# Kernel optimization log

Hardware: AMD Instinct MI355X
Metric: run time of the kernel (lower is better)

Reference implementation:

```python
import jax, jax.numpy as jnp
import numpy as np

NUM_HEADS = 16
HEAD_DIM = 128
D_MODEL = 2048
BATCH = 2
SEQ = 2048


def setup_inputs() -> dict:
    key = jax.random.key(0)
    ks = jax.random.split(key, 6)
    x = jax.random.normal(ks[0], (BATCH, SEQ, D_MODEL), dtype=jnp.float32)
    # RoPE tables (real/imag parts of freqs_cis), shape [S, HEAD_DIM//2]
    pos = jnp.arange(SEQ, dtype=jnp.float32)[:, None]
    inv_freq = 1.0 / (10000.0 ** (jnp.arange(0, HEAD_DIM, 2, dtype=jnp.float32) / HEAD_DIM))
    ang = pos * inv_freq[None, :]
    freq_cos = jnp.cos(ang)
    freq_sin = jnp.sin(ang)
    scale = 1.0 / np.sqrt(D_MODEL)
    wq = jax.random.normal(ks[1], (D_MODEL, NUM_HEADS * HEAD_DIM), dtype=jnp.float32) * scale
    wk = jax.random.normal(ks[2], (D_MODEL, NUM_HEADS * HEAD_DIM), dtype=jnp.float32) * scale
    wv = jax.random.normal(ks[3], (D_MODEL, NUM_HEADS * HEAD_DIM), dtype=jnp.float32) * scale
    wo = jax.random.normal(ks[4], (NUM_HEADS * HEAD_DIM, D_MODEL), dtype=jnp.float32) * scale
    return {"x": x, "freq_cos": freq_cos, "freq_sin": freq_sin,
            "wq": wq, "wk": wk, "wv": wv, "wo": wo}


def _rotate_half(t):
    half = t.shape[-1] // 2
    return jnp.concatenate([-t[..., half:], t[..., :half]], axis=-1)


def _apply_rope(q, k, freq_cos, freq_sin):
    # q, k: [B, H, S, D]; freq_cos/sin: [S_total, D//2]
    q = q.astype(jnp.float32)
    k = k.astype(jnp.float32)
    S = q.shape[2]
    cos = jnp.concatenate([freq_cos[:S], freq_cos[:S]], axis=-1)[None, None]  # [1,1,S,D]
    sin = jnp.concatenate([freq_sin[:S], freq_sin[:S]], axis=-1)[None, None]
    q_out = q * cos + _rotate_half(q) * sin
    k_out = k * cos + _rotate_half(k) * sin
    return q_out, k_out


def reference(x, freq_cos, freq_sin, wq, wk, wv, wo):
    B, S, D = x.shape
    H, hd = NUM_HEADS, HEAD_DIM
    q = (x @ wq).reshape(B, S, H, hd).transpose(0, 2, 1, 3)  # [B,H,S,hd]
    k = (x @ wk).reshape(B, S, H, hd).transpose(0, 2, 1, 3)
    v = (x @ wv).reshape(B, S, H, hd).transpose(0, 2, 1, 3)
    q, k = _apply_rope(q, k, freq_cos, freq_sin)
    # explicit causal attention (faithful to CPU/GPU path)
    logits = jnp.einsum('bhqd,bhkd->bhqk', q, k) / jnp.sqrt(jnp.float32(hd))
    mask = jnp.tril(jnp.ones((S, S), dtype=jnp.float32))
    logits = jnp.where(mask[None, None, :, :], logits, -1e10)
    weights = jax.nn.softmax(logits, axis=-1)
    out = jnp.einsum('bhqk,bhkd->bhqd', weights, v)  # [B,H,S,hd]
    out = out.transpose(0, 2, 1, 3).reshape(B, S, H * hd)
    return out @ wo
```

## Files before the change

kernel.cpp:

```cpp
#include <hip/hip_runtime.h>

typedef unsigned short u16;
typedef unsigned int u32;
typedef __attribute__((ext_vector_type(8))) short bf16x8;
typedef __attribute__((ext_vector_type(4))) short bf16x4;
typedef __attribute__((ext_vector_type(4))) float f32x4;

#define MFMA(a, b, c) __builtin_amdgcn_mfma_f32_16x16x32_bf16(a, b, c, 0, 0, 0)
#define ASYNC16(g, l)                                                        \
  __builtin_amdgcn_global_load_lds(                                          \
      (const __attribute__((address_space(1))) u32*)(g),                     \
      (__attribute__((address_space(3))) u32*)(l), 16, 0, 0)

__device__ __forceinline__ float b2f(u16 u) {
  union { u32 i; float f; } x; x.i = ((u32)u) << 16; return x.f;
}
__device__ __forceinline__ u16 f2b(float f) {
  union { float f; u32 i; } x; x.f = f;
  return (u16)((x.i + 0x7fff + ((x.i >> 16) & 1)) >> 16);
}
__device__ __forceinline__ f32x4 fzero4() { f32x4 z = {0.f, 0.f, 0.f, 0.f}; return z; }

__global__ __launch_bounds__(256) void cvt_x(const float* __restrict__ src,
                                             u16* __restrict__ dst) {
  const int i = (blockIdx.x * 256 + threadIdx.x) * 4;
  const f32x4 v = *(const f32x4*)(src + i);
  bf16x4 o;
  o[0] = (short)f2b(v[0]); o[1] = (short)f2b(v[1]);
  o[2] = (short)f2b(v[2]); o[3] = (short)f2b(v[3]);
  *(bf16x4*)(dst + i) = o;
}

__global__ __launch_bounds__(256) void wtrans_f32(const float* __restrict__ src,
                                                  u16* __restrict__ dst) {
  __shared__ u16 tile[64][65];
  const int k0 = blockIdx.y * 64, n0 = blockIdx.x * 64;
  const int t = threadIdx.x;
  const int tr = t >> 3, tc = t & 7;

#pragma unroll
  for (int hh = 0; hh < 2; ++hh) {
    const int k = tr + hh * 32;
    const float* p = src + (size_t)(k0 + k) * 2048 + n0 + tc * 8;
    const f32x4 a = *(const f32x4*)(p);
    const f32x4 b = *(const f32x4*)(p + 4);
#pragma unroll
    for (int j = 0; j < 4; ++j) tile[k][tc * 8 + j] = f2b(a[j]);
#pragma unroll
    for (int j = 0; j < 4; ++j) tile[k][tc * 8 + 4 + j] = f2b(b[j]);
  }
  __syncthreads();
#pragma unroll
  for (int hh = 0; hh < 2; ++hh) {
    const int n = tr + hh * 32;
    bf16x8 v;
#pragma unroll
    for (int j = 0; j < 8; ++j) v[j] = (short)tile[tc * 8 + j][n];
    *(bf16x8*)(dst + (size_t)(n0 + n) * 2048 + k0 + tc * 8) = v;
  }
}

__global__ __launch_bounds__(256) void wtrans3(const float* __restrict__ wq,
                                               const float* __restrict__ wk,
                                               const float* __restrict__ wv,
                                               u16* __restrict__ wTall) {
  __shared__ u16 tile[64][65];
  const int z = blockIdx.z;
  const float* src = (z == 0) ? wq : (z == 1) ? wk : wv;
  u16* dst = wTall + (size_t)z * 2048 * 2048;
  const int k0 = blockIdx.y * 64, n0 = blockIdx.x * 64;
  const int t = threadIdx.x;
  const int tr = t >> 3, tc = t & 7;

#pragma unroll
  for (int hh = 0; hh < 2; ++hh) {
    const int k = tr + hh * 32;
    const float* p = src + (size_t)(k0 + k) * 2048 + n0 + tc * 8;
    const f32x4 a = *(const f32x4*)(p);
    const f32x4 b = *(const f32x4*)(p + 4);
#pragma unroll
    for (int j = 0; j < 4; ++j) tile[k][tc * 8 + j] = f2b(a[j]);
#pragma unroll
    for (int j = 0; j < 4; ++j) tile[k][tc * 8 + 4 + j] = f2b(b[j]);
  }
  __syncthreads();
#pragma unroll
  for (int hh = 0; hh < 2; ++hh) {
    const int n = tr + hh * 32;
    bf16x8 v;
#pragma unroll
    for (int j = 0; j < 8; ++j) v[j] = (short)tile[tc * 8 + j][n];
    *(bf16x8*)(dst + (size_t)(n0 + n) * 2048 + k0 + tc * 8) = v;
  }
}

__device__ __forceinline__ void gemm_mainloop(const u16* __restrict__ A,
                                              const u16* __restrict__ Bt,
                                              int K, int m0, int n0,
                                              u16* lA, u16* lB,
                                              f32x4 acc[4][4]) {
  const int tid = threadIdx.x;
  const int lane = tid & 63;
  const int wave = tid >> 6;
  const int quad = lane >> 4;
  const int l16 = lane & 15;
  const int wr = wave >> 1, wc = wave & 1;

  const int srow = lane >> 2;
  const int scol = (lane & 3) * 8;
  const u16* ga0 = A + (size_t)(m0 + (wave * 2 + 0) * 16 + srow) * K + scol;
  const u16* ga1 = A + (size_t)(m0 + (wave * 2 + 1) * 16 + srow) * K + scol;
  const u16* gb0 = Bt + (size_t)(n0 + (wave * 2 + 0) * 16 + srow) * K + scol;
  const u16* gb1 = Bt + (size_t)(n0 + (wave * 2 + 1) * 16 + srow) * K + scol;
  u16* la0 = lA + (wave * 2 + 0) * 512;
  u16* la1 = lA + (wave * 2 + 1) * 512;
  u16* lb0 = lB + (wave * 2 + 0) * 512;
  u16* lb1 = lB + (wave * 2 + 1) * 512;

  for (int k0 = 0; k0 < K; k0 += 32) {
    ASYNC16(ga0 + k0, la0);
    ASYNC16(ga1 + k0, la1);
    ASYNC16(gb0 + k0, lb0);
    ASYNC16(gb1 + k0, lb1);
    __syncthreads();
    bf16x8 af[4], bfr[4];
#pragma unroll
    for (int mb = 0; mb < 4; ++mb)
      af[mb] = *(const bf16x8*)(lA + ((wr * 64 + mb * 16 + l16) * 32 + quad * 8));
#pragma unroll
    for (int nb = 0; nb < 4; ++nb)
      bfr[nb] = *(const bf16x8*)(lB + ((wc * 64 + nb * 16 + l16) * 32 + quad * 8));
#pragma unroll
    for (int mb = 0; mb < 4; ++mb)
#pragma unroll
      for (int nb = 0; nb < 4; ++nb)
        acc[mb][nb] = MFMA(af[mb], bfr[nb], acc[mb][nb]);
    __syncthreads();
  }
}

__global__ __launch_bounds__(256) void gemm_qkv(const u16* __restrict__ x,
                                                const u16* __restrict__ wT,
                                                u16* __restrict__ qkv) {
  __shared__ u16 lA[128 * 32];
  __shared__ u16 lB[128 * 32];
  f32x4 acc[4][4];
#pragma unroll
  for (int i = 0; i < 4; ++i)
#pragma unroll
    for (int j = 0; j < 4; ++j) acc[i][j] = fzero4();

  const int m0 = blockIdx.y * 128, n0 = blockIdx.x * 128;
  gemm_mainloop(x, wT, 2048, m0, n0, lA, lB, acc);

  const int lane = threadIdx.x & 63, wave = threadIdx.x >> 6;
  const int quad = lane >> 4, l16 = lane & 15;
  const int wr = wave >> 1, wc = wave & 1;
#pragma unroll
  for (int mb = 0; mb < 4; ++mb)
#pragma unroll
    for (int nb = 0; nb < 4; ++nb)
#pragma unroll
      for (int r = 0; r < 4; ++r) {
        const int row = m0 + wr * 64 + mb * 16 + quad * 4 + r;
        const int col = n0 + wc * 64 + nb * 16 + l16;
        const int b = row >> 11, s = row & 2047;
        const int which = col >> 11, rem = col & 2047;
        const int hh = rem >> 7, d = rem & 127;
        const size_t idx = (size_t)which * ((size_t)4096 * 2048) +
                           (((size_t)(b * 16 + hh) * 2048 + s) * 128 + d);
        qkv[idx] = f2b(acc[mb][nb][r]);
      }
}

__global__ __launch_bounds__(256) void gemm_out(const u16* __restrict__ Oin,
                                                const u16* __restrict__ woT,
                                                float* __restrict__ out) {
  __shared__ u16 lA[128 * 32];
  __shared__ u16 lB[128 * 32];
  f32x4 acc[4][4];
#pragma unroll
  for (int i = 0; i < 4; ++i)
#pragma unroll
    for (int j = 0; j < 4; ++j) acc[i][j] = fzero4();

  const int m0 = blockIdx.y * 128, n0 = blockIdx.x * 128;
  gemm_mainloop(Oin, woT, 2048, m0, n0, lA, lB, acc);

  const int lane = threadIdx.x & 63, wave = threadIdx.x >> 6;
  const int quad = lane >> 4, l16 = lane & 15;
  const int wr = wave >> 1, wc = wave & 1;
#pragma unroll
  for (int mb = 0; mb < 4; ++mb)
#pragma unroll
    for (int nb = 0; nb < 4; ++nb)
#pragma unroll
      for (int r = 0; r < 4; ++r) {
        const int row = m0 + wr * 64 + mb * 16 + quad * 4 + r;
        const int col = n0 + wc * 64 + nb * 16 + l16;
        out[(size_t)row * 2048 + col] = acc[mb][nb][r];
      }
}

__global__ __launch_bounds__(256) void rope_kernel(u16* __restrict__ Q,
                                                   u16* __restrict__ K,
                                                   const float* __restrict__ fcos,
                                                   const float* __restrict__ fsin) {
  const int i = blockIdx.x * 256 + threadIdx.x;
  const int d = i & 63;
  const int s = (i >> 6) & 2047;
  const int bh = i >> 17;
  const size_t base = ((size_t)bh * 2048 + s) * 128;
  const float c = fcos[s * 64 + d];
  const float sn = fsin[s * 64 + d];
  const float qs = 0.08838834764831845f;

  const float q0 = b2f(Q[base + d]), q1 = b2f(Q[base + d + 64]);
  Q[base + d] = f2b((q0 * c - q1 * sn) * qs);
  Q[base + d + 64] = f2b((q1 * c + q0 * sn) * qs);
  const float k0 = b2f(K[base + d]), k1 = b2f(K[base + d + 64]);
  K[base + d] = f2b(k0 * c - k1 * sn);
  K[base + d + 64] = f2b(k1 * c + k0 * sn);
}

__global__ __launch_bounds__(256) void attn2(const u16* __restrict__ Q,
                                             const u16* __restrict__ K,
                                             const u16* __restrict__ V,
                                             u16* __restrict__ O) {
  __shared__ u16 lK[64 * 136];
  __shared__ u16 lV[128 * 72];
  __shared__ u16 lP[4 * 16 * 72];

  const int bh = blockIdx.y;
  const int b = bh >> 4, h = bh & 15;
  const u16* Qh = Q + (size_t)bh * 2048 * 128;
  const u16* Kh = K + (size_t)bh * 2048 * 128;
  const u16* Vh = V + (size_t)bh * 2048 * 128;

  const int tid = threadIdx.x;
  const int lane = tid & 63, wave = tid >> 6;
  const int quad = lane >> 4, l16 = lane & 15;
  const int np = tid & 31, dg = tid >> 5;
  const int d0 = dg * 16, r0 = np * 2;
  const int krow = tid >> 4, kj = tid & 15;
  u16* lPw = lP + wave * (16 * 72);

  bf16x8 kreg[4], vreg[4];

#pragma unroll
  for (int half = 0; half < 2; ++half) {
    const int qt = (half == 0) ? (int)blockIdx.x : 31 - (int)blockIdx.x;
    const int q0 = qt * 64;

    bf16x8 qf[4];
    {
      const u16* qrow = Qh + (size_t)(q0 + wave * 16 + l16) * 128 + quad * 8;
#pragma unroll
      for (int kc = 0; kc < 4; ++kc) qf[kc] = *(const bf16x8*)(qrow + kc * 32);
    }

    float m_i[4], l_i[4];
    f32x4 accO[8];
#pragma unroll
    for (int r = 0; r < 4; ++r) { m_i[r] = -1e30f; l_i[r] = 0.f; }
#pragma unroll
    for (int db = 0; db < 8; ++db) accO[db] = fzero4();

    {
#pragma unroll
      for (int i = 0; i < 4; ++i)
        kreg[i] = *(const bf16x8*)(Kh + (size_t)(krow + 16 * i) * 128 + kj * 8);
      const u16* vp = Vh + (size_t)r0 * 128 + d0;
      vreg[0] = *(const bf16x8*)(vp);
      vreg[1] = *(const bf16x8*)(vp + 8);
      vreg[2] = *(const bf16x8*)(vp + 128);
      vreg[3] = *(const bf16x8*)(vp + 136);
    }

    for (int n0 = 0; n0 <= q0; n0 += 64) {
#pragma unroll
      for (int i = 0; i < 4; ++i)
        *(bf16x8*)(lK + (krow + 16 * i) * 136 + kj * 8) = kreg[i];
#pragma unroll
      for (int j = 0; j < 8; ++j) {
        const u32 lo = (u16)vreg[0][j], hi = (u16)vreg[2][j];
        *(u32*)(lV + (d0 + j) * 72 + r0) = lo | (hi << 16);
      }
#pragma unroll
      for (int j = 0; j < 8; ++j) {
        const u32 lo = (u16)vreg[1][j], hi = (u16)vreg[3][j];
        *(u32*)(lV + (d0 + 8 + j) * 72 + r0) = lo | (hi << 16);
      }
      __syncthreads();

      if (n0 + 64 <= q0) {
        const int nn = n0 + 64;
#pragma unroll
        for (int i = 0; i < 4; ++i)
          kreg[i] = *(const bf16x8*)(Kh + (size_t)(nn + krow + 16 * i) * 128 + kj * 8);
        const u16* vp = Vh + (size_t)(nn + r0) * 128 + d0;
        vreg[0] = *(const bf16x8*)(vp);
        vreg[1] = *(const bf16x8*)(vp + 8);
        vreg[2] = *(const bf16x8*)(vp + 128);
        vreg[3] = *(const bf16x8*)(vp + 136);
      }

      f32x4 sf[4];
#pragma unroll
      for (int nb = 0; nb < 4; ++nb) {
        sf[nb] = fzero4();
#pragma unroll
        for (int kc = 0; kc < 4; ++kc) {
          bf16x8 kf = *(const bf16x8*)(lK + ((nb * 16 + l16) * 136 + kc * 32 + quad * 8));
          sf[nb] = MFMA(qf[kc], kf, sf[nb]);
        }
      }
      if (n0 == q0) {
#pragma unroll
        for (int nb = 0; nb < 4; ++nb)
#pragma unroll
          for (int r = 0; r < 4; ++r) {
            const int rowl = wave * 16 + quad * 4 + r;
            const int coll = nb * 16 + l16;
            if (coll > rowl) sf[nb][r] = -1e30f;
          }
      }
      float pr[4][4], alpha[4];
#pragma unroll
      for (int r = 0; r < 4; ++r) {
        float mx = fmaxf(fmaxf(sf[0][r], sf[1][r]), fmaxf(sf[2][r], sf[3][r]));
#pragma unroll
        for (int off = 1; off < 16; off <<= 1) mx = fmaxf(mx, __shfl_xor(mx, off));
        const float mn = fmaxf(m_i[r], mx);
        alpha[r] = __expf(m_i[r] - mn);
        m_i[r] = mn;
        float rs = 0.f;
#pragma unroll
        for (int nb = 0; nb < 4; ++nb) {
          const float p = __expf(sf[nb][r] - mn);
          pr[nb][r] = p;
          rs += p;
        }
#pragma unroll
        for (int off = 1; off < 16; off <<= 1) rs += __shfl_xor(rs, off);
        l_i[r] = l_i[r] * alpha[r] + rs;
      }
#pragma unroll
      for (int db = 0; db < 8; ++db)
#pragma unroll
        for (int r = 0; r < 4; ++r) accO[db][r] *= alpha[r];

#pragma unroll
      for (int nb = 0; nb < 4; ++nb)
#pragma unroll
        for (int r = 0; r < 4; ++r)
          lPw[(quad * 4 + r) * 72 + nb * 16 + l16] = f2b(pr[nb][r]);
      __syncthreads();

#pragma unroll
      for (int kc2 = 0; kc2 < 2; ++kc2) {
        bf16x8 pf = *(const bf16x8*)(lPw + (l16 * 72 + kc2 * 32 + quad * 8));
#pragma unroll
        for (int db = 0; db < 8; ++db) {
          bf16x8 vf = *(const bf16x8*)(lV + ((db * 16 + l16) * 72 + kc2 * 32 + quad * 8));
          accO[db] = MFMA(pf, vf, accO[db]);
        }
      }
      __syncthreads();
    }

#pragma unroll
    for (int r = 0; r < 4; ++r) {
      const float inv = 1.0f / l_i[r];
      const int srow = q0 + wave * 16 + quad * 4 + r;
      u16* orow = O + ((size_t)b * 2048 + srow) * 2048 + h * 128;
#pragma unroll
      for (int db = 0; db < 8; ++db)
        orow[db * 16 + l16] = f2b(accO[db][r] * inv);
    }
  }
}

extern "C" void kernel_launch(void* const* d_in, const int* in_sizes, int n_in,
                              void* d_out, int out_size, void* d_ws, size_t ws_size,
                              hipStream_t stream) {
  const float* x  = (const float*)d_in[0];
  const float* fc = (const float*)d_in[1];
  const float* fs = (const float*)d_in[2];
  const float* wq = (const float*)d_in[3];
  const float* wk = (const float*)d_in[4];
  const float* wv = (const float*)d_in[5];
  const float* wo = (const float*)d_in[6];
  float* out = (float*)d_out;

  u16* ws = (u16*)d_ws;
  const size_t BUF = (size_t)4096 * 2048;
  u16* xb  = ws;
  u16* Ob  = ws;
  u16* Qb  = ws + 1 * BUF;
  u16* Kb  = ws + 2 * BUF;
  u16* Vb  = ws + 3 * BUF;
  u16* wTall = (u16*)d_out;
  u16* woT = Kb;

  hipLaunchKernelGGL(cvt_x, dim3(8192), dim3(256), 0, stream, x, xb);
  hipLaunchKernelGGL(wtrans3, dim3(32, 32, 3), dim3(256), 0, stream, wq, wk, wv, wTall);
  hipLaunchKernelGGL(gemm_qkv, dim3(48, 32), dim3(256), 0, stream, xb, wTall, Qb);
  hipLaunchKernelGGL(rope_kernel, dim3(16384), dim3(256), 0, stream, Qb, Kb, fc, fs);
  hipLaunchKernelGGL(attn2, dim3(16, 32), dim3(256), 0, stream, Qb, Kb, Vb, Ob);
  hipLaunchKernelGGL(wtrans_f32, dim3(32, 32), dim3(256), 0, stream, wo, woT);
  hipLaunchKernelGGL(gemm_out, dim3(16, 32), dim3(256), 0, stream, Ob, woT, out);
}
```

Baseline: 421.6 us.

## Rewrite QKV GEMM with 256x256 tiles, 4-stage async LDS pipeline, XCD swizzle

Replaces the 128x128 single-buffered QKV projection GEMM with a 512-thread kernel that computes 256x256 tiles. It uses a 4-deep ring of global_load_lds stages, split A/B prefetch interleaved with MFMA phases, raised priority around the MFMA blocks, and a block-index remap that groups tiles per XCD. The goal is to hide global-load latency behind matrix math, raise arithmetic intensity per tile, and improve L2 locality. The cost is 128KB of LDS per block, which lowers occupancy, plus hand-written vmcnt waits that must stay in step with the stage count.

```diff
diff --git a/kernel.cpp b/kernel.cpp
--- a/kernel.cpp
+++ b/kernel.cpp
@@ -11,6 +11,13 @@
   __builtin_amdgcn_global_load_lds(                                          \
       (const __attribute__((address_space(1))) u32*)(g),                     \
       (__attribute__((address_space(3))) u32*)(l), 16, 0, 0)
+
+#define SBARRIER()                                                           \
+  do {                                                                       \
+    asm volatile("" ::: "memory");                                           \
+    __builtin_amdgcn_s_barrier();                                            \
+    asm volatile("" ::: "memory");                                           \
+  } while (0)
 
 __device__ __forceinline__ float b2f(u16 u) {
   union { u32 i; float f; } x; x.i = ((u32)u) << 16; return x.f;
@@ -139,35 +146,118 @@
   }
 }
 
-__global__ __launch_bounds__(256) void gemm_qkv(const u16* __restrict__ x,
-                                                const u16* __restrict__ wT,
-                                                u16* __restrict__ qkv) {
-  __shared__ u16 lA[128 * 32];
-  __shared__ u16 lB[128 * 32];
-  f32x4 acc[4][4];
-#pragma unroll
-  for (int i = 0; i < 4; ++i)
+__global__ __launch_bounds__(512, 2) void gemm_qkv2(const u16* __restrict__ A,
+                                                    const u16* __restrict__ Bt,
+                                                    u16* __restrict__ qkv) {
+  __shared__ u16 lA[4 * 8192];
+  __shared__ u16 lB[4 * 8192];
+
+  const int orig = blockIdx.x;
+  const int wg = (orig & 7) * 48 + (orig >> 3);
+  const int m0 = (wg / 24) * 256;
+  const int n0 = (wg % 24) * 256;
+
+  const int tid = threadIdx.x;
+  const int lane = tid & 63;
+  const int wave = tid >> 6;
+  const int quad = lane >> 4, l16 = lane & 15;
+  const int wr = wave >> 2, wc = wave & 3;
+
+  const int srow = tid & 255;
+  const int sq = tid >> 8;
+  const u16* gA = A + (size_t)(m0 + srow) * 2048 + sq * 8;
+  const u16* gB = Bt + (size_t)(n0 + srow) * 2048 + sq * 8;
+  const int ldst = wave * 512;
+
+#define STAGE_A(t)                                                           \
+  do {                                                                       \
+    u16* d_ = lA + (((t) & 3) << 13) + ldst;                                 \
+    ASYNC16(gA + (t) * 32, d_);                                              \
+    ASYNC16(gA + (t) * 32 + 16, d_ + 4096);                                  \
+  } while (0)
+#define STAGE_B(t)                                                           \
+  do {                                                                       \
+    u16* d_ = lB + (((t) & 3) << 13) + ldst;                                 \
+    ASYNC16(gB + (t) * 32, d_);                                              \
+    ASYNC16(gB + (t) * 32 + 16, d_ + 4096);                                  \
+  } while (0)
+
+  f32x4 acc[8][4];
+#pragma unroll
+  for (int i = 0; i < 8; ++i)
 #pragma unroll
     for (int j = 0; j < 4; ++j) acc[i][j] = fzero4();
 
-  const int m0 = blockIdx.y * 128, n0 = blockIdx.x * 128;
-  gemm_mainloop(x, wT, 2048, m0, n0, lA, lB, acc);
-
-  const int lane = threadIdx.x & 63, wave = threadIdx.x >> 6;
-  const int quad = lane >> 4, l16 = lane & 15;
-  const int wr = wave >> 1, wc = wave & 1;
-#pragma unroll
-  for (int mb = 0; mb < 4; ++mb)
+  STAGE_A(0); STAGE_B(0);
+  STAGE_A(1); STAGE_B(1);
+  STAGE_A(2); STAGE_B(2);
+  asm volatile("s_waitcnt vmcnt(8)" ::: "memory");
+  SBARRIER();
+
+  const int aoff = wr * 128 + l16;
+  const int boff = wc * 64 + l16;
+
+  for (int t = 0; t < 64; ++t) {
+    const u16* sA = lA + ((t & 3) << 13) + quad * 2048;
+    const u16* sB = lB + ((t & 3) << 13) + quad * 2048;
+
+    bf16x8 af[4], bfr[4];
+#pragma unroll
+    for (int mb = 0; mb < 4; ++mb)
+      af[mb] = *(const bf16x8*)(sA + (aoff + mb * 16) * 8);
 #pragma unroll
     for (int nb = 0; nb < 4; ++nb)
+      bfr[nb] = *(const bf16x8*)(sB + (boff + nb * 16) * 8);
+    if (t <= 60) STAGE_A(t + 3);
+    SBARRIER();
+    asm volatile("s_waitcnt lgkmcnt(0)" ::: "memory");
+    __builtin_amdgcn_s_setprio(1);
+#pragma unroll
+    for (int mb = 0; mb < 4; ++mb)
+#pragma unroll
+      for (int nb = 0; nb < 4; ++nb)
+        acc[mb][nb] = MFMA(af[mb], bfr[nb], acc[mb][nb]);
+    __builtin_amdgcn_s_setprio(0);
+    SBARRIER();
+
+#pragma unroll
+    for (int mb = 0; mb < 4; ++mb)
+      af[mb] = *(const bf16x8*)(sA + (aoff + (mb + 4) * 16) * 8);
+    if (t <= 60) STAGE_B(t + 3);
+    SBARRIER();
+    asm volatile("s_waitcnt lgkmcnt(0)" ::: "memory");
+    __builtin_amdgcn_s_setprio(1);
+#pragma unroll
+    for (int mb = 0; mb < 4; ++mb)
+#pragma unroll
+      for (int nb = 0; nb < 4; ++nb)
+        acc[mb + 4][nb] = MFMA(af[mb], bfr[nb], acc[mb + 4][nb]);
+    __builtin_amdgcn_s_setprio(0);
+    if (t < 61) {
+      asm volatile("s_waitcnt vmcnt(8)" ::: "memory");
+    } else if (t == 61) {
+      asm volatile("s_waitcnt vmcnt(4)" ::: "memory");
+    } else if (t == 62) {
+      asm volatile("s_waitcnt vmcnt(0)" ::: "memory");
+    }
+    SBARRIER();
+  }
+#undef STAGE_A
+#undef STAGE_B
+
+  const size_t BUF = (size_t)4096 * 2048;
+#pragma unroll
+  for (int mb = 0; mb < 8; ++mb)
+#pragma unroll
+    for (int nb = 0; nb < 4; ++nb)
 #pragma unroll
       for (int r = 0; r < 4; ++r) {
-        const int row = m0 + wr * 64 + mb * 16 + quad * 4 + r;
+        const int row = m0 + wr * 128 + mb * 16 + quad * 4 + r;
         const int col = n0 + wc * 64 + nb * 16 + l16;
         const int b = row >> 11, s = row & 2047;
         const int which = col >> 11, rem = col & 2047;
         const int hh = rem >> 7, d = rem & 127;
-        const size_t idx = (size_t)which * ((size_t)4096 * 2048) +
+        const size_t idx = (size_t)which * BUF +
                            (((size_t)(b * 16 + hh) * 2048 + s) * 128 + d);
         qkv[idx] = f2b(acc[mb][nb][r]);
       }
@@ -405,7 +495,7 @@
 
   hipLaunchKernelGGL(cvt_x, dim3(8192), dim3(256), 0, stream, x, xb);
   hipLaunchKernelGGL(wtrans3, dim3(32, 32, 3), dim3(256), 0, stream, wq, wk, wv, wTall);
-  hipLaunchKernelGGL(gemm_qkv, dim3(48, 32), dim3(256), 0, stream, xb, wTall, Qb);
+  hipLaunchKernelGGL(gemm_qkv2, dim3(384), dim3(512), 0, stream, xb, wTall, Qb);
   hipLaunchKernelGGL(rope_kernel, dim3(16384), dim3(256), 0, stream, Qb, Kb, fc, fs);
   hipLaunchKernelGGL(attn2, dim3(16, 32), dim3(256), 0, stream, Qb, Kb, Vb, Ob);
   hipLaunchKernelGGL(wtrans_f32, dim3(32, 32), dim3(256), 0, stream, wo, woT);
```

New measurement: 467.8 us. +11.0%, slower.

## Double attention KV tile to 128 rows and skip fully masked blocks

Applied to the files above, without the earlier changes.

The causal attention kernel now processes 128 keys per iteration instead of 64. This halves the number of LDS staging rounds and block barriers per query tile. Score blocks that lie entirely above the diagonal are skipped rather than computed and masked. The barrier between writing P to shared memory and reading it back is removed, which is safe because each wave has its own P buffer. The trade-off is more shared memory per block, more registers for the prefetched K/V and score fragments, and a `launch_bounds` hint asking for two blocks per CU.

```diff
diff --git a/kernel.cpp b/kernel.cpp
--- a/kernel.cpp
+++ b/kernel.cpp
@@ -223,12 +223,12 @@
   K[base + d + 64] = f2b(k1 * c + k0 * sn);
 }
 
-__global__ __launch_bounds__(256) void attn2(const u16* __restrict__ Q,
-                                             const u16* __restrict__ K,
-                                             const u16* __restrict__ V,
-                                             u16* __restrict__ O) {
-  __shared__ u16 lK[64 * 136];
-  __shared__ u16 lV[128 * 72];
+__global__ __launch_bounds__(256, 2) void attn3(const u16* __restrict__ Q,
+                                                const u16* __restrict__ K,
+                                                const u16* __restrict__ V,
+                                                u16* __restrict__ O) {
+  __shared__ u16 lK[128 * 136];
+  __shared__ u16 lV[128 * 132];
   __shared__ u16 lP[4 * 16 * 72];
 
   const int bh = blockIdx.y;
@@ -240,12 +240,11 @@
   const int tid = threadIdx.x;
   const int lane = tid & 63, wave = tid >> 6;
   const int quad = lane >> 4, l16 = lane & 15;
-  const int np = tid & 31, dg = tid >> 5;
-  const int d0 = dg * 16, r0 = np * 2;
   const int krow = tid >> 4, kj = tid & 15;
+  const int r0 = (tid & 63) * 2, d0 = (tid >> 6) * 32;
   u16* lPw = lP + wave * (16 * 72);
 
-  bf16x8 kreg[4], vreg[4];
+  bf16x8 kreg[8], vreg[8];
 
 #pragma unroll
   for (int half = 0; half < 2; ++half) {
@@ -268,67 +267,75 @@
 
     {
 #pragma unroll
-      for (int i = 0; i < 4; ++i)
+      for (int i = 0; i < 8; ++i)
         kreg[i] = *(const bf16x8*)(Kh + (size_t)(krow + 16 * i) * 128 + kj * 8);
       const u16* vp = Vh + (size_t)r0 * 128 + d0;
-      vreg[0] = *(const bf16x8*)(vp);
-      vreg[1] = *(const bf16x8*)(vp + 8);
-      vreg[2] = *(const bf16x8*)(vp + 128);
-      vreg[3] = *(const bf16x8*)(vp + 136);
+#pragma unroll
+      for (int c = 0; c < 4; ++c) {
+        vreg[c] = *(const bf16x8*)(vp + c * 8);
+        vreg[4 + c] = *(const bf16x8*)(vp + 128 + c * 8);
+      }
     }
 
-    for (int n0 = 0; n0 <= q0; n0 += 64) {
-#pragma unroll
-      for (int i = 0; i < 4; ++i)
+    for (int n0 = 0; n0 <= q0; n0 += 128) {
+#pragma unroll
+      for (int i = 0; i < 8; ++i)
         *(bf16x8*)(lK + (krow + 16 * i) * 136 + kj * 8) = kreg[i];
 #pragma unroll
-      for (int j = 0; j < 8; ++j) {
-        const u32 lo = (u16)vreg[0][j], hi = (u16)vreg[2][j];
-        *(u32*)(lV + (d0 + j) * 72 + r0) = lo | (hi << 16);
-      }
-#pragma unroll
-      for (int j = 0; j < 8; ++j) {
-        const u32 lo = (u16)vreg[1][j], hi = (u16)vreg[3][j];
-        *(u32*)(lV + (d0 + 8 + j) * 72 + r0) = lo | (hi << 16);
-      }
+      for (int c = 0; c < 4; ++c)
+#pragma unroll
+        for (int j = 0; j < 8; ++j) {
+          const u32 lo = (u16)vreg[c][j], hi = (u16)vreg[4 + c][j];
+          *(u32*)(lV + (d0 + c * 8 + j) * 132 + r0) = lo | (hi << 16);
+        }
       __syncthreads();
 
-      if (n0 + 64 <= q0) {
-        const int nn = n0 + 64;
-#pragma unroll
-        for (int i = 0; i < 4; ++i)
+      if (n0 + 128 <= q0) {
+        const int nn = n0 + 128;
+#pragma unroll
+        for (int i = 0; i < 8; ++i)
           kreg[i] = *(const bf16x8*)(Kh + (size_t)(nn + krow + 16 * i) * 128 + kj * 8);
         const u16* vp = Vh + (size_t)(nn + r0) * 128 + d0;
-        vreg[0] = *(const bf16x8*)(vp);
-        vreg[1] = *(const bf16x8*)(vp + 8);
-        vreg[2] = *(const bf16x8*)(vp + 128);
-        vreg[3] = *(const bf16x8*)(vp + 136);
-      }
-
-      f32x4 sf[4];
-#pragma unroll
-      for (int nb = 0; nb < 4; ++nb) {
-        sf[nb] = fzero4();
-#pragma unroll
-        for (int kc = 0; kc < 4; ++kc) {
-          bf16x8 kf = *(const bf16x8*)(lK + ((nb * 16 + l16) * 136 + kc * 32 + quad * 8));
-          sf[nb] = MFMA(qf[kc], kf, sf[nb]);
+#pragma unroll
+        for (int c = 0; c < 4; ++c) {
+          vreg[c] = *(const bf16x8*)(vp + c * 8);
+          vreg[4 + c] = *(const bf16x8*)(vp + 128 + c * 8);
         }
       }
-      if (n0 == q0) {
-#pragma unroll
-        for (int nb = 0; nb < 4; ++nb)
+
+      f32x4 sf[8];
+      const int nbLim = (q0 + 64 - n0) >> 4;
+#pragma unroll
+      for (int nb = 0; nb < 8; ++nb) {
+        if (nb < nbLim) {
+          sf[nb] = fzero4();
+#pragma unroll
+          for (int kc = 0; kc < 4; ++kc) {
+            bf16x8 kf = *(const bf16x8*)(lK + ((nb * 16 + l16) * 136 + kc * 32 + quad * 8));
+            sf[nb] = MFMA(qf[kc], kf, sf[nb]);
+          }
+        } else {
+          sf[nb][0] = -1e30f; sf[nb][1] = -1e30f;
+          sf[nb][2] = -1e30f; sf[nb][3] = -1e30f;
+        }
+      }
+      if (n0 + 128 > q0) {
+#pragma unroll
+        for (int nb = 0; nb < 8; ++nb)
 #pragma unroll
           for (int r = 0; r < 4; ++r) {
-            const int rowl = wave * 16 + quad * 4 + r;
-            const int coll = nb * 16 + l16;
-            if (coll > rowl) sf[nb][r] = -1e30f;
+            const int rowg = q0 + wave * 16 + quad * 4 + r;
+            const int colg = n0 + nb * 16 + l16;
+            if (colg > rowg) sf[nb][r] = -1e30f;
           }
       }
-      float pr[4][4], alpha[4];
+
+      float alpha[4];
 #pragma unroll
       for (int r = 0; r < 4; ++r) {
-        float mx = fmaxf(fmaxf(sf[0][r], sf[1][r]), fmaxf(sf[2][r], sf[3][r]));
+        float mx = sf[0][r];
+#pragma unroll
+        for (int nb = 1; nb < 8; ++nb) mx = fmaxf(mx, sf[nb][r]);
 #pragma unroll
         for (int off = 1; off < 16; off <<= 1) mx = fmaxf(mx, __shfl_xor(mx, off));
         const float mn = fmaxf(m_i[r], mx);
@@ -336,9 +343,9 @@
         m_i[r] = mn;
         float rs = 0.f;
 #pragma unroll
-        for (int nb = 0; nb < 4; ++nb) {
+        for (int nb = 0; nb < 8; ++nb) {
           const float p = __expf(sf[nb][r] - mn);
-          pr[nb][r] = p;
+          sf[nb][r] = p;
           rs += p;
         }
 #pragma unroll
@@ -350,20 +357,28 @@
 #pragma unroll
         for (int r = 0; r < 4; ++r) accO[db][r] *= alpha[r];
 
+      bf16x8 pf[4];
 #pragma unroll
       for (int nb = 0; nb < 4; ++nb)
 #pragma unroll
         for (int r = 0; r < 4; ++r)
-          lPw[(quad * 4 + r) * 72 + nb * 16 + l16] = f2b(pr[nb][r]);
-      __syncthreads();
-
-#pragma unroll
-      for (int kc2 = 0; kc2 < 2; ++kc2) {
-        bf16x8 pf = *(const bf16x8*)(lPw + (l16 * 72 + kc2 * 32 + quad * 8));
+          lPw[(quad * 4 + r) * 72 + nb * 16 + l16] = f2b(sf[nb][r]);
+      pf[0] = *(const bf16x8*)(lPw + (l16 * 72 + quad * 8));
+      pf[1] = *(const bf16x8*)(lPw + (l16 * 72 + 32 + quad * 8));
+#pragma unroll
+      for (int nb = 0; nb < 4; ++nb)
+#pragma unroll
+        for (int r = 0; r < 4; ++r)
+          lPw[(quad * 4 + r) * 72 + nb * 16 + l16] = f2b(sf[nb + 4][r]);
+      pf[2] = *(const bf16x8*)(lPw + (l16 * 72 + quad * 8));
+      pf[3] = *(const bf16x8*)(lPw + (l16 * 72 + 32 + quad * 8));
+
+#pragma unroll
+      for (int kc2 = 0; kc2 < 4; ++kc2) {
 #pragma unroll
         for (int db = 0; db < 8; ++db) {
-          bf16x8 vf = *(const bf16x8*)(lV + ((db * 16 + l16) * 72 + kc2 * 32 + quad * 8));
-          accO[db] = MFMA(pf, vf, accO[db]);
+          bf16x8 vf = *(const bf16x8*)(lV + ((db * 16 + l16) * 132 + kc2 * 32 + quad * 8));
+          accO[db] = MFMA(pf[kc2], vf, accO[db]);
         }
       }
       __syncthreads();
@@ -407,7 +422,7 @@
   hipLaunchKernelGGL(wtrans3, dim3(32, 32, 3), dim3(256), 0, stream, wq, wk, wv, wTall);
   hipLaunchKernelGGL(gemm_qkv, dim3(48, 32), dim3(256), 0, stream, xb, wTall, Qb);
   hipLaunchKernelGGL(rope_kernel, dim3(16384), dim3(256), 0, stream, Qb, Kb, fc, fs);
-  hipLaunchKernelGGL(attn2, dim3(16, 32), dim3(256), 0, stream, Qb, Kb, Vb, Ob);
+  hipLaunchKernelGGL(attn3, dim3(16, 32), dim3(256), 0, stream, Qb, Kb, Vb, Ob);
   hipLaunchKernelGGL(wtrans_f32, dim3(32, 32), dim3(256), 0, stream, wo, woT);
   hipLaunchKernelGGL(gemm_out, dim3(16, 32), dim3(256), 0, stream, Ob, woT, out);
 }
```

Result: no change. 418.9 us (-0.7%).

## Rewrite attention with 32x32 MFMA, register-resident P, and 128-row query tiles

Applied to the files above, without the earlier changes.

Replaces the attention kernel with one that uses 32x32x16 bf16 MFMA. Scores are computed transposed (K times Q), so softmax needs only a cross-half lane shuffle instead of 16-lane reductions. P stays in registers, packed with a bf16 conversion instruction and swapped between lane halves, which removes the LDS round-trip and one barrier per tile. Each block handles one 128-row query tile with a reordered block-to-head mapping and launch bounds set for two blocks per CU. This gives up the old per-block pairing of a short and a long causal tile, risking load imbalance, and adds alpha/l shuffles for the transposed layout.

```diff
diff --git a/kernel.cpp b/kernel.cpp
--- a/kernel.cpp
+++ b/kernel.cpp
@@ -5,8 +5,10 @@
 typedef __attribute__((ext_vector_type(8))) short bf16x8;
 typedef __attribute__((ext_vector_type(4))) short bf16x4;
 typedef __attribute__((ext_vector_type(4))) float f32x4;
+typedef __attribute__((ext_vector_type(16))) float f32x16;
 
 #define MFMA(a, b, c) __builtin_amdgcn_mfma_f32_16x16x32_bf16(a, b, c, 0, 0, 0)
+#define MFMA32(a, b, c) __builtin_amdgcn_mfma_f32_32x32x16_bf16(a, b, c, 0, 0, 0)
 #define ASYNC16(g, l)                                                        \
   __builtin_amdgcn_global_load_lds(                                          \
       (const __attribute__((address_space(1))) u32*)(g),                     \
@@ -20,6 +22,17 @@
   return (u16)((x.i + 0x7fff + ((x.i >> 16) & 1)) >> 16);
 }
 __device__ __forceinline__ f32x4 fzero4() { f32x4 z = {0.f, 0.f, 0.f, 0.f}; return z; }
+__device__ __forceinline__ f32x16 fzero16() {
+  f32x16 z;
+#pragma unroll
+  for (int i = 0; i < 16; ++i) z[i] = 0.f;
+  return z;
+}
+__device__ __forceinline__ u32 pkbf16(float lo, float hi) {
+  u32 r;
+  asm("v_cvt_pk_bf16_f32 %0, %1, %2" : "=v"(r) : "v"(lo), "v"(hi));
+  return r;
+}
 
 __global__ __launch_bounds__(256) void cvt_x(const float* __restrict__ src,
                                              u16* __restrict__ dst) {
@@ -223,15 +236,76 @@
   K[base + d + 64] = f2b(k1 * c + k0 * sn);
 }
 
-__global__ __launch_bounds__(256) void attn2(const u16* __restrict__ Q,
-                                             const u16* __restrict__ K,
-                                             const u16* __restrict__ V,
-                                             u16* __restrict__ O) {
+template <int NB>
+__device__ __forceinline__ void qkt_block(f32x16& sv, int n0, int qlo, int hi,
+                                          int c, const u16* lK,
+                                          const bf16x8* qf) {
+  const int lo = n0 + NB * 32;
+  if (lo < qlo + 32) {
+    sv = fzero16();
+#pragma unroll
+    for (int kc = 0; kc < 8; ++kc) {
+      const bf16x8 kf =
+          *(const bf16x8*)(lK + (NB * 32 + c) * 136 + kc * 16 + hi * 8);
+      sv = MFMA32(kf, qf[kc], sv);
+    }
+    if (lo == qlo) {
+#pragma unroll
+      for (int r = 0; r < 16; ++r) {
+        const int n32 = (r & 3) + 8 * (r >> 2) + 4 * hi;
+        if (n32 > c) sv[r] = -1e30f;
+      }
+    }
+  } else {
+#pragma unroll
+    for (int r = 0; r < 16; ++r) sv[r] = -1e30f;
+  }
+}
+
+template <int NB>
+__device__ __forceinline__ void pv_block(const f32x16& sv, int n0, int qlo,
+                                         int hi, int c, const u16* lV,
+                                         f32x16* accO) {
+  if (n0 + NB * 32 < qlo + 32) {
+#pragma unroll
+    for (int half = 0; half < 2; ++half) {
+      const int rb = half * 8;
+      const u32 pA = pkbf16(sv[rb + 0], sv[rb + 1]);
+      const u32 pB = pkbf16(sv[rb + 2], sv[rb + 3]);
+      const u32 pC = pkbf16(sv[rb + 4], sv[rb + 5]);
+      const u32 pD = pkbf16(sv[rb + 6], sv[rb + 7]);
+      const u32 xA = (u32)__shfl_xor((int)pA, 32);
+      const u32 xB = (u32)__shfl_xor((int)pB, 32);
+      const u32 xC = (u32)__shfl_xor((int)pC, 32);
+      const u32 xD = (u32)__shfl_xor((int)pD, 32);
+      bf16x8 pa;
+      u32* pw = (u32*)&pa;
+      pw[0] = hi ? xC : pA;
+      pw[1] = hi ? xD : pB;
+      pw[2] = hi ? pC : xA;
+      pw[3] = hi ? pD : xB;
+#pragma unroll
+      for (int db = 0; db < 4; ++db) {
+        const bf16x8 vf = *(const bf16x8*)(lV + (db * 32 + c) * 72 +
+                                           NB * 32 + half * 16 + hi * 8);
+        accO[db] = MFMA32(pa, vf, accO[db]);
+      }
+    }
+  }
+}
+
+__global__ __launch_bounds__(256, 2) void attn4(const u16* __restrict__ Q,
+                                                const u16* __restrict__ K,
+                                                const u16* __restrict__ V,
+                                                u16* __restrict__ O) {
   __shared__ u16 lK[64 * 136];
   __shared__ u16 lV[128 * 72];
-  __shared__ u16 lP[4 * 16 * 72];
-
-  const int bh = blockIdx.y;
+
+  const int bid = blockIdx.x;
+  const int bh = (bid & 7) + 8 * ((bid >> 3) & 3);
+  const int tq = bid >> 5;
+  const int qt = (tq < 8) ? tq : 23 - tq;
+  const int q0 = qt * 128;
   const int b = bh >> 4, h = bh & 15;
   const u16* Qh = Q + (size_t)bh * 2048 * 128;
   const u16* Kh = K + (size_t)bh * 2048 * 128;
@@ -239,145 +313,111 @@
 
   const int tid = threadIdx.x;
   const int lane = tid & 63, wave = tid >> 6;
-  const int quad = lane >> 4, l16 = lane & 15;
-  const int np = tid & 31, dg = tid >> 5;
-  const int d0 = dg * 16, r0 = np * 2;
+  const int hi = lane >> 5, c = lane & 31;
+  const int qlo = q0 + wave * 32;
   const int krow = tid >> 4, kj = tid & 15;
-  u16* lPw = lP + wave * (16 * 72);
+  const int r0 = (tid & 31) * 2, d0v = (tid >> 5) * 16;
+
+  bf16x8 qf[8];
+  {
+    const u16* qrow = Qh + (size_t)(q0 + wave * 32 + c) * 128 + hi * 8;
+#pragma unroll
+    for (int kc = 0; kc < 8; ++kc) qf[kc] = *(const bf16x8*)(qrow + kc * 16);
+  }
+
+  float m_i = -1e30f, l_i = 0.f;
+  f32x16 accO[4];
+#pragma unroll
+  for (int db = 0; db < 4; ++db) accO[db] = fzero16();
+
+  const int nIter = 2 * qt + 2;
 
   bf16x8 kreg[4], vreg[4];
-
-#pragma unroll
-  for (int half = 0; half < 2; ++half) {
-    const int qt = (half == 0) ? (int)blockIdx.x : 31 - (int)blockIdx.x;
-    const int q0 = qt * 64;
-
-    bf16x8 qf[4];
-    {
-      const u16* qrow = Qh + (size_t)(q0 + wave * 16 + l16) * 128 + quad * 8;
-#pragma unroll
-      for (int kc = 0; kc < 4; ++kc) qf[kc] = *(const bf16x8*)(qrow + kc * 32);
-    }
-
-    float m_i[4], l_i[4];
-    f32x4 accO[8];
-#pragma unroll
-    for (int r = 0; r < 4; ++r) { m_i[r] = -1e30f; l_i[r] = 0.f; }
-#pragma unroll
-    for (int db = 0; db < 8; ++db) accO[db] = fzero4();
-
-    {
+  {
+#pragma unroll
+    for (int i = 0; i < 4; ++i)
+      kreg[i] = *(const bf16x8*)(Kh + (size_t)(krow + 16 * i) * 128 + kj * 8);
+    const u16* vp = Vh + (size_t)r0 * 128 + d0v;
+    vreg[0] = *(const bf16x8*)(vp);
+    vreg[1] = *(const bf16x8*)(vp + 8);
+    vreg[2] = *(const bf16x8*)(vp + 128);
+    vreg[3] = *(const bf16x8*)(vp + 136);
+  }
+
+  for (int it = 0; it < nIter; ++it) {
+    const int n0 = it * 64;
+#pragma unroll
+    for (int i = 0; i < 4; ++i)
+      *(bf16x8*)(lK + (krow + 16 * i) * 136 + kj * 8) = kreg[i];
+#pragma unroll
+    for (int j = 0; j < 8; ++j) {
+      const u32 lo = (u16)vreg[0][j], hi2 = (u16)vreg[2][j];
+      *(u32*)(lV + (d0v + j) * 72 + r0) = lo | (hi2 << 16);
+    }
+#pragma unroll
+    for (int j = 0; j < 8; ++j) {
+      const u32 lo = (u16)vreg[1][j], hi2 = (u16)vreg[3][j];
+      *(u32*)(lV + (d0v + 8 + j) * 72 + r0) = lo | (hi2 << 16);
+    }
+    __syncthreads();
+
+    if (it + 1 < nIter) {
+      const int nn = n0 + 64;
 #pragma unroll
       for (int i = 0; i < 4; ++i)
-        kreg[i] = *(const bf16x8*)(Kh + (size_t)(krow + 16 * i) * 128 + kj * 8);
-      const u16* vp = Vh + (size_t)r0 * 128 + d0;
+        kreg[i] =
+            *(const bf16x8*)(Kh + (size_t)(nn + krow + 16 * i) * 128 + kj * 8);
+      const u16* vp = Vh + (size_t)(nn + r0) * 128 + d0v;
       vreg[0] = *(const bf16x8*)(vp);
       vreg[1] = *(const bf16x8*)(vp + 8);
       vreg[2] = *(const bf16x8*)(vp + 128);
       vreg[3] = *(const bf16x8*)(vp + 136);
     }
 
-    for (int n0 = 0; n0 <= q0; n0 += 64) {
-#pragma unroll
-      for (int i = 0; i < 4; ++i)
-        *(bf16x8*)(lK + (krow + 16 * i) * 136 + kj * 8) = kreg[i];
-#pragma unroll
-      for (int j = 0; j < 8; ++j) {
-        const u32 lo = (u16)vreg[0][j], hi = (u16)vreg[2][j];
-        *(u32*)(lV + (d0 + j) * 72 + r0) = lo | (hi << 16);
-      }
-#pragma unroll
-      for (int j = 0; j < 8; ++j) {
-        const u32 lo = (u16)vreg[1][j], hi = (u16)vreg[3][j];
-        *(u32*)(lV + (d0 + 8 + j) * 72 + r0) = lo | (hi << 16);
-      }
-      __syncthreads();
-
-      if (n0 + 64 <= q0) {
-        const int nn = n0 + 64;
-#pragma unroll
-        for (int i = 0; i < 4; ++i)
-          kreg[i] = *(const bf16x8*)(Kh + (size_t)(nn + krow + 16 * i) * 128 + kj * 8);
-        const u16* vp = Vh + (size_t)(nn + r0) * 128 + d0;
-        vreg[0] = *(const bf16x8*)(vp);
-        vreg[1] = *(const bf16x8*)(vp + 8);
-        vreg[2] = *(const bf16x8*)(vp + 128);
-        vreg[3] = *(const bf16x8*)(vp + 136);
-      }
-
-      f32x4 sf[4];
-#pragma unroll
-      for (int nb = 0; nb < 4; ++nb) {
-        sf[nb] = fzero4();
-#pragma unroll
-        for (int kc = 0; kc < 4; ++kc) {
-          bf16x8 kf = *(const bf16x8*)(lK + ((nb * 16 + l16) * 136 + kc * 32 + quad * 8));
-          sf[nb] = MFMA(qf[kc], kf, sf[nb]);
-        }
-      }
-      if (n0 == q0) {
-#pragma unroll
-        for (int nb = 0; nb < 4; ++nb)
-#pragma unroll
-          for (int r = 0; r < 4; ++r) {
-            const int rowl = wave * 16 + quad * 4 + r;
-            const int coll = nb * 16 + l16;
-            if (coll > rowl) sf[nb][r] = -1e30f;
-          }
-      }
-      float pr[4][4], alpha[4];
-#pragma unroll
-      for (int r = 0; r < 4; ++r) {
-        float mx = fmaxf(fmaxf(sf[0][r], sf[1][r]), fmaxf(sf[2][r], sf[3][r]));
-#pragma unroll
-        for (int off = 1; off < 16; off <<= 1) mx = fmaxf(mx, __shfl_xor(mx, off));
-        const float mn = fmaxf(m_i[r], mx);
-        alpha[r] = __expf(m_i[r] - mn);
-        m_i[r] = mn;
-        float rs = 0.f;
-#pragma unroll
-        for (int nb = 0; nb < 4; ++nb) {
-          const float p = __expf(sf[nb][r] - mn);
-          pr[nb][r] = p;
-          rs += p;
-        }
-#pragma unroll
-        for (int off = 1; off < 16; off <<= 1) rs += __shfl_xor(rs, off);
-        l_i[r] = l_i[r] * alpha[r] + rs;
-      }
-#pragma unroll
-      for (int db = 0; db < 8; ++db)
-#pragma unroll
-        for (int r = 0; r < 4; ++r) accO[db][r] *= alpha[r];
-
-#pragma unroll
-      for (int nb = 0; nb < 4; ++nb)
-#pragma unroll
-        for (int r = 0; r < 4; ++r)
-          lPw[(quad * 4 + r) * 72 + nb * 16 + l16] = f2b(pr[nb][r]);
-      __syncthreads();
-
-#pragma unroll
-      for (int kc2 = 0; kc2 < 2; ++kc2) {
-        bf16x8 pf = *(const bf16x8*)(lPw + (l16 * 72 + kc2 * 32 + quad * 8));
-#pragma unroll
-        for (int db = 0; db < 8; ++db) {
-          bf16x8 vf = *(const bf16x8*)(lV + ((db * 16 + l16) * 72 + kc2 * 32 + quad * 8));
-          accO[db] = MFMA(pf, vf, accO[db]);
-        }
-      }
-      __syncthreads();
-    }
-
-#pragma unroll
-    for (int r = 0; r < 4; ++r) {
-      const float inv = 1.0f / l_i[r];
-      const int srow = q0 + wave * 16 + quad * 4 + r;
-      u16* orow = O + ((size_t)b * 2048 + srow) * 2048 + h * 128;
-#pragma unroll
-      for (int db = 0; db < 8; ++db)
-        orow[db * 16 + l16] = f2b(accO[db][r] * inv);
-    }
+    f32x16 s0, s1;
+    qkt_block<0>(s0, n0, qlo, hi, c, lK, qf);
+    qkt_block<1>(s1, n0, qlo, hi, c, lK, qf);
+
+    float mx = -1e30f;
+#pragma unroll
+    for (int r = 0; r < 16; ++r) mx = fmaxf(mx, fmaxf(s0[r], s1[r]));
+    mx = fmaxf(mx, __shfl_xor(mx, 32));
+    const float mn = fmaxf(m_i, mx);
+    const float alpha = __expf(m_i - mn);
+    m_i = mn;
+    float rs = 0.f;
+#pragma unroll
+    for (int r = 0; r < 16; ++r) {
+      const float p0 = __expf(s0[r] - mn);
+      const float p1 = __expf(s1[r] - mn);
+      s0[r] = p0; s1[r] = p1;
+      rs += p0 + p1;
+    }
+    rs += __shfl_xor(rs, 32);
+    l_i = l_i * alpha + rs;
+
+#pragma unroll
+    for (int r = 0; r < 16; ++r) {
+      const int src = ((r & 3) + 8 * (r >> 2) + 4 * hi) + (lane & 32);
+      const float aa = __shfl(alpha, src);
+      accO[0][r] *= aa; accO[1][r] *= aa;
+      accO[2][r] *= aa; accO[3][r] *= aa;
+    }
+
+    pv_block<0>(s0, n0, qlo, hi, c, lV, accO);
+    pv_block<1>(s1, n0, qlo, hi, c, lV, accO);
+    __syncthreads();
+  }
+
+  const float linv = 1.f / l_i;
+#pragma unroll
+  for (int r = 0; r < 16; ++r) {
+    const int q32 = (r & 3) + 8 * (r >> 2) + 4 * hi;
+    const float inv = __shfl(linv, q32 + (lane & 32));
+    const int srow = q0 + wave * 32 + q32;
+    u16* orow = O + ((size_t)b * 2048 + srow) * 2048 + h * 128 + c;
+#pragma unroll
+    for (int db = 0; db < 4; ++db) orow[db * 32] = f2b(accO[db][r] * inv);
   }
 }
 
@@ -407,7 +447,7 @@
   hipLaunchKernelGGL(wtrans3, dim3(32, 32, 3), dim3(256), 0, stream, wq, wk, wv, wTall);
   hipLaunchKernelGGL(gemm_qkv, dim3(48, 32), dim3(256), 0, stream, xb, wTall, Qb);
   hipLaunchKernelGGL(rope_kernel, dim3(16384), dim3(256), 0, stream, Qb, Kb, fc, fs);
-  hipLaunchKernelGGL(attn2, dim3(16, 32), dim3(256), 0, stream, Qb, Kb, Vb, Ob);
+  hipLaunchKernelGGL(attn4, dim3(512), dim3(256), 0, stream, Qb, Kb, Vb, Ob);
   hipLaunchKernelGGL(wtrans_f32, dim3(32, 32), dim3(256), 0, stream, wo, woT);
   hipLaunchKernelGGL(gemm_out, dim3(16, 32), dim3(256), 0, stream, Ob, woT, out);
 }
```

New measurement: 393.5 us. 1.07x faster.
